# Performance work log

Measured on AMD Instinct MI355X. Metric: run time of the kernel, lower is better.

The kernel has to match this reference:

```python
import jax, jax.numpy as jnp
import numpy as np

LN_EPS = 1e-5


def layer_norm(h, gamma, beta):
    m = jnp.mean(h, axis=-1, keepdims=True)
    v = jnp.mean((h - m) ** 2, axis=-1, keepdims=True)
    return (h - m) * jax.lax.rsqrt(v + LN_EPS) * gamma + beta


def setup_inputs() -> dict:
    key = jax.random.key(0)
    ks = jax.random.split(key, 4)
    B, N, D, H = 4, 256, 256, 256
    x = jax.random.normal(ks[0], (B, N, D), dtype=jnp.float32)
    # Linear(2D, H): weight stored as (in, out) for x @ W
    Wg = jax.random.normal(ks[1], (2 * D, H), dtype=jnp.float32) * (1.0 / np.sqrt(2 * D))
    bg = jnp.zeros((H,), dtype=jnp.float32)
    g_gamma = jnp.ones((H,), dtype=jnp.float32)
    g_beta = jnp.zeros((H,), dtype=jnp.float32)
    Wf = jax.random.normal(ks[2], (H, H), dtype=jnp.float32) * (1.0 / np.sqrt(H))
    bf = jnp.zeros((H,), dtype=jnp.float32)
    f_gamma = jnp.ones((H,), dtype=jnp.float32)
    f_beta = jnp.zeros((H,), dtype=jnp.float32)
    return {"x": x, "Wg": Wg, "bg": bg, "g_gamma": g_gamma, "g_beta": g_beta,
            "Wf": Wf, "bf": bf, "f_gamma": f_gamma, "f_beta": f_beta}


def reference(x, Wg, bg, g_gamma, g_beta, Wf, bf, f_gamma, f_beta):
    B, N, D = x.shape
    # Linear on concat([xi, xj]) == xi @ Wg[:D] + xj @ Wg[D:] ; avoids the (B,N,N,2D) cat.
    a = jnp.einsum('bnd,dh->bnh', x, Wg[:D])   # i-part
    b = jnp.einsum('bnd,dh->bnh', x, Wg[D:])   # j-part
    # pair pre-activation: (B, N_i, N_j, H)
    pre = a[:, :, None, :] + b[:, None, :, :] + bg
    r = layer_norm(jax.nn.relu(pre), g_gamma, g_beta)
    r = jnp.sum(r, axis=(1, 2))                # (B, H)
    rel = layer_norm(jax.nn.relu(r @ Wf + bf), f_gamma, f_beta)  # (B, H)
    return rel[:, None, :] + x                 # broadcast over N
```

## Files before the change

### kernel.cpp

```cpp
#include <hip/hip_runtime.h>

#define LN_EPS 1e-5f

constexpr int Bn = 4, Nn = 256, Dn = 256, Hn = 256;

__global__ __launch_bounds__(256) void gemm_ab_kernel(
    const float* __restrict__ x, const float* __restrict__ Wg,
    const float* __restrict__ bg, float* __restrict__ aA, float* __restrict__ bB)
{
    int mt = blockIdx.x;
    int half = blockIdx.y;
    int m0 = mt * 8;
    int t = threadIdx.x;
    __shared__ float xs[8][256];
    const float4* xsrc = reinterpret_cast<const float4*>(x + m0 * Dn);
    float4* xdst = reinterpret_cast<float4*>(&xs[0][0]);
    for (int k = t; k < 512; k += 256) xdst[k] = xsrc[k];
    __syncthreads();
    int h = t;
    const float* W = Wg + (half ? Dn * Hn : 0) + h;
    float acc[8];
    float binit = half ? 0.0f : bg[h];
#pragma unroll
    for (int mm = 0; mm < 8; ++mm) acc[mm] = binit;
    for (int d = 0; d < 256; d += 4) {
        float w0 = W[(d + 0) * Hn];
        float w1 = W[(d + 1) * Hn];
        float w2 = W[(d + 2) * Hn];
        float w3 = W[(d + 3) * Hn];
#pragma unroll
        for (int mm = 0; mm < 8; ++mm) {
            float4 xv = *reinterpret_cast<const float4*>(&xs[mm][d]);
            acc[mm] = fmaf(xv.x, w0, acc[mm]);
            acc[mm] = fmaf(xv.y, w1, acc[mm]);
            acc[mm] = fmaf(xv.z, w2, acc[mm]);
            acc[mm] = fmaf(xv.w, w3, acc[mm]);
        }
    }
    float* outp = half ? bB : aA;
#pragma unroll
    for (int mm = 0; mm < 8; ++mm) outp[(m0 + mm) * Hn + h] = acc[mm];
}

__global__ __launch_bounds__(512) void pair_kernel(
    const float* __restrict__ aA, const float* __restrict__ bB,
    float* __restrict__ part)
{
    int b  = blockIdx.x >> 6;
    int i0 = (blockIdx.x & 63) * 4;
    int t = threadIdx.x;
    __shared__ float A[4][256];
    __shared__ float2 invd[4][256];

    for (int k = t; k < 1024; k += 512)
        A[k >> 8][k & 255] = aA[(b * Nn + i0 + (k >> 8)) * Hn + (k & 255)];
    __syncthreads();

    int j = t & 255;
    int g = t >> 8;

    {
        float s0 = 0.f, s1 = 0.f, q0 = 0.f, q1 = 0.f;
        const float* brow = bB + (b * Nn + j) * Hn;
        const float* A0 = A[2 * g];
        const float* A1 = A[2 * g + 1];
#pragma unroll 2
        for (int h = 0; h < 256; h += 4) {
            float4 bb = *reinterpret_cast<const float4*>(brow + h);
            float4 a0 = *reinterpret_cast<const float4*>(A0 + h);
            float4 a1 = *reinterpret_cast<const float4*>(A1 + h);
            float v;
            v = fmaxf(a0.x + bb.x, 0.f); s0 += v; q0 = fmaf(v, v, q0);
            v = fmaxf(a0.y + bb.y, 0.f); s0 += v; q0 = fmaf(v, v, q0);
            v = fmaxf(a0.z + bb.z, 0.f); s0 += v; q0 = fmaf(v, v, q0);
            v = fmaxf(a0.w + bb.w, 0.f); s0 += v; q0 = fmaf(v, v, q0);
            v = fmaxf(a1.x + bb.x, 0.f); s1 += v; q1 = fmaf(v, v, q1);
            v = fmaxf(a1.y + bb.y, 0.f); s1 += v; q1 = fmaf(v, v, q1);
            v = fmaxf(a1.z + bb.z, 0.f); s1 += v; q1 = fmaf(v, v, q1);
            v = fmaxf(a1.w + bb.w, 0.f); s1 += v; q1 = fmaf(v, v, q1);
        }
        float m0 = s0 * (1.f / 256.f);
        float m1 = s1 * (1.f / 256.f);
        float inv0 = rsqrtf(q0 * (1.f / 256.f) - m0 * m0 + LN_EPS);
        float inv1 = rsqrtf(q1 * (1.f / 256.f) - m1 * m1 + LN_EPS);
        invd[2 * g][j]     = make_float2(inv0, -m0 * inv0);
        invd[2 * g + 1][j] = make_float2(inv1, -m1 * inv1);
    }
    __syncthreads();

    int h = t & 255;
    float a0 = A[2 * g][h];
    float a1 = A[2 * g + 1][h];
    float acc0 = 0.f, acc1 = 0.f;
    const float* bcol = bB + b * Nn * Hn + h;
#pragma unroll 4
    for (int j2 = 0; j2 < 256; ++j2) {
        float bb = bcol[j2 * Hn];
        float2 id0 = invd[2 * g][j2];
        float2 id1 = invd[2 * g + 1][j2];
        float v0 = fmaxf(a0 + bb, 0.f);
        float v1 = fmaxf(a1 + bb, 0.f);
        acc0 += fmaf(id0.x, v0, id0.y);
        acc1 += fmaf(id1.x, v1, id1.y);
    }
    part[(b * Nn + i0 + 2 * g) * Hn + h]     = acc0;
    part[(b * Nn + i0 + 2 * g + 1) * Hn + h] = acc1;
}

__global__ __launch_bounds__(1024) void finish_kernel(
    const float* __restrict__ part,
    const float* __restrict__ gg, const float* __restrict__ gb,
    const float* __restrict__ Wf, const float* __restrict__ bfv,
    const float* __restrict__ fg, const float* __restrict__ fb,
    float* __restrict__ rel)
{
    int b = blockIdx.x;
    int t = threadIdx.x;
    int h = t & 255;
    int q = t >> 8;

    __shared__ float psum[4][256];
    __shared__ float rs[256];
    __shared__ float ysum[4][256];
    __shared__ float pS[16], pQ[16];

    float s = 0.f;
    const float* p = part + (b * Nn + q * 64) * Hn + h;
#pragma unroll 4
    for (int i = 0; i < 64; ++i) s += p[i * Hn];
    psum[q][h] = s;
    __syncthreads();

    if (q == 0) {
        float rsum = psum[0][h] + psum[1][h] + psum[2][h] + psum[3][h];
        rs[h] = gg[h] * rsum + 65536.0f * gb[h];
    }
    __syncthreads();

    float y = 0.f;
    const float* Wcol = Wf + (q * 64) * Hn + h;
#pragma unroll 4
    for (int k = 0; k < 64; ++k) y = fmaf(rs[q * 64 + k], Wcol[k * Hn], y);
    ysum[q][h] = y;
    __syncthreads();

    float v = fmaxf(ysum[0][h] + ysum[1][h] + ysum[2][h] + ysum[3][h] + bfv[h], 0.f);

    float sv = v, qv = v * v;
#pragma unroll
    for (int off = 32; off >= 1; off >>= 1) {
        sv += __shfl_xor(sv, off, 64);
        qv += __shfl_xor(qv, off, 64);
    }
    int wid = t >> 6, lane = t & 63;
    if (lane == 0) { pS[wid] = sv; pQ[wid] = qv; }
    __syncthreads();
    float S = 0.f, Q = 0.f;
#pragma unroll
    for (int w = 0; w < 16; ++w) { S += pS[w]; Q += pQ[w]; }
    float m = S * (1.f / 1024.f);
    float var = Q * (1.f / 1024.f) - m * m;
    float inv = rsqrtf(var + LN_EPS);

    if (q == 0)
        rel[b * Hn + h] = (v - m) * inv * fg[h] + fb[h];
}

__global__ __launch_bounds__(256) void add_kernel(
    const float* __restrict__ rel, const float* __restrict__ x,
    float* __restrict__ out)
{
    int idx = blockIdx.x * blockDim.x + threadIdx.x;
    int b = idx >> 14;
    int d4 = idx & 63;
    float4 r4 = reinterpret_cast<const float4*>(rel)[b * 64 + d4];
    float4 x4 = reinterpret_cast<const float4*>(x)[idx];
    float4 o;
    o.x = r4.x + x4.x;
    o.y = r4.y + x4.y;
    o.z = r4.z + x4.z;
    o.w = r4.w + x4.w;
    reinterpret_cast<float4*>(out)[idx] = o;
}

extern "C" void kernel_launch(void* const* d_in, const int* in_sizes, int n_in,
                              void* d_out, int out_size, void* d_ws, size_t ws_size,
                              hipStream_t stream)
{
    const float* x   = (const float*)d_in[0];
    const float* Wg  = (const float*)d_in[1];
    const float* bg  = (const float*)d_in[2];
    const float* gg  = (const float*)d_in[3];
    const float* gb  = (const float*)d_in[4];
    const float* Wf  = (const float*)d_in[5];
    const float* bfv = (const float*)d_in[6];
    const float* fg  = (const float*)d_in[7];
    const float* fb  = (const float*)d_in[8];
    float* out = (float*)d_out;

    float* ws   = (float*)d_ws;
    float* aA   = ws;
    float* bB   = ws + 262144;
    float* part = ws + 524288;
    float* rel  = ws + 786432;

    gemm_ab_kernel<<<dim3(128, 2), 256, 0, stream>>>(x, Wg, bg, aA, bB);
    pair_kernel<<<256, 512, 0, stream>>>(aA, bB, part);
    finish_kernel<<<4, 1024, 0, stream>>>(part, gg, gb, Wf, bfv, fg, fb, rel);
    add_kernel<<<256, 256, 0, stream>>>(rel, x, out);
}
```

Before: 125.5 us.

## Transpose b into workspace, atomically reduce pair sums, shrink GEMM tiles

The GEMM kernel now also writes a transposed copy of b, so the pair kernel's per-j statistics pass reads b with coalesced column-major loads instead of strided rows. The per-pair LayerNorm offset term is folded into a single per-batch scalar accumulated with atomics. Per-block partial sums are atomically added into a small reduction buffer, replacing the large partial array that finish_kernel had to reduce. The GEMM tile is halved to 4 rows to double the block count, and the inner loop is unrolled by 8. This trades an extra strided write of b in the GEMM and atomic contention for less memory traffic and less finish work. It also relies on gemm block 0 zeroing the accumulator before later kernels run, and float atomics make the summation order nondeterministic.

```diff
diff --git a/kernel.cpp b/kernel.cpp
--- a/kernel.cpp
+++ b/kernel.cpp
@@ -3,54 +3,76 @@
 #define LN_EPS 1e-5f
 
 constexpr int Bn = 4, Nn = 256, Dn = 256, Hn = 256;
+
 
 __global__ __launch_bounds__(256) void gemm_ab_kernel(
     const float* __restrict__ x, const float* __restrict__ Wg,
-    const float* __restrict__ bg, float* __restrict__ aA, float* __restrict__ bB)
+    const float* __restrict__ bg, float* __restrict__ aA,
+    float* __restrict__ bB, float* __restrict__ bBt, float* __restrict__ rC)
 {
     int mt = blockIdx.x;
     int half = blockIdx.y;
-    int m0 = mt * 8;
+    int m0 = mt * 4;
     int t = threadIdx.x;
-    __shared__ float xs[8][256];
+
+    if (mt == 0 && half == 0) {
+        for (int k = t; k < 1028; k += 256) rC[k] = 0.0f;
+    }
+
+    __shared__ float xs[4][256];
     const float4* xsrc = reinterpret_cast<const float4*>(x + m0 * Dn);
-    float4* xdst = reinterpret_cast<float4*>(&xs[0][0]);
-    for (int k = t; k < 512; k += 256) xdst[k] = xsrc[k];
-    __syncthreads();
+    reinterpret_cast<float4*>(&xs[0][0])[t] = xsrc[t];
+    __syncthreads();
+
     int h = t;
     const float* W = Wg + (half ? Dn * Hn : 0) + h;
-    float acc[8];
     float binit = half ? 0.0f : bg[h];
-#pragma unroll
-    for (int mm = 0; mm < 8; ++mm) acc[mm] = binit;
-    for (int d = 0; d < 256; d += 4) {
+    float acc[4] = {binit, binit, binit, binit};
+
+    for (int d = 0; d < 256; d += 8) {
         float w0 = W[(d + 0) * Hn];
         float w1 = W[(d + 1) * Hn];
         float w2 = W[(d + 2) * Hn];
         float w3 = W[(d + 3) * Hn];
-#pragma unroll
-        for (int mm = 0; mm < 8; ++mm) {
-            float4 xv = *reinterpret_cast<const float4*>(&xs[mm][d]);
-            acc[mm] = fmaf(xv.x, w0, acc[mm]);
-            acc[mm] = fmaf(xv.y, w1, acc[mm]);
-            acc[mm] = fmaf(xv.z, w2, acc[mm]);
-            acc[mm] = fmaf(xv.w, w3, acc[mm]);
+        float w4 = W[(d + 4) * Hn];
+        float w5 = W[(d + 5) * Hn];
+        float w6 = W[(d + 6) * Hn];
+        float w7 = W[(d + 7) * Hn];
+#pragma unroll
+        for (int mm = 0; mm < 4; ++mm) {
+            float4 xa = *reinterpret_cast<const float4*>(&xs[mm][d]);
+            float4 xb = *reinterpret_cast<const float4*>(&xs[mm][d + 4]);
+            float a = acc[mm];
+            a = fmaf(xa.x, w0, a); a = fmaf(xa.y, w1, a);
+            a = fmaf(xa.z, w2, a); a = fmaf(xa.w, w3, a);
+            a = fmaf(xb.x, w4, a); a = fmaf(xb.y, w5, a);
+            a = fmaf(xb.z, w6, a); a = fmaf(xb.w, w7, a);
+            acc[mm] = a;
         }
     }
-    float* outp = half ? bB : aA;
-#pragma unroll
-    for (int mm = 0; mm < 8; ++mm) outp[(m0 + mm) * Hn + h] = acc[mm];
+
+    if (half == 0) {
+#pragma unroll
+        for (int mm = 0; mm < 4; ++mm) aA[(m0 + mm) * Hn + h] = acc[mm];
+    } else {
+#pragma unroll
+        for (int mm = 0; mm < 4; ++mm) bB[(m0 + mm) * Hn + h] = acc[mm];
+        int b = m0 >> 8, i0 = m0 & 255;
+        float4 v = make_float4(acc[0], acc[1], acc[2], acc[3]);
+        *reinterpret_cast<float4*>(&bBt[(b * Hn + h) * Nn + i0]) = v;
+    }
 }
 
 __global__ __launch_bounds__(512) void pair_kernel(
     const float* __restrict__ aA, const float* __restrict__ bB,
-    float* __restrict__ part)
+    const float* __restrict__ bBt, float* __restrict__ rC)
 {
     int b  = blockIdx.x >> 6;
     int i0 = (blockIdx.x & 63) * 4;
     int t = threadIdx.x;
     __shared__ float A[4][256];
-    __shared__ float2 invd[4][256];
+    __shared__ float invL[4][256];
+    __shared__ float red[2][256];
 
     for (int k = t; k < 1024; k += 512)
         A[k >> 8][k & 255] = aA[(b * Nn + i0 + (k >> 8)) * Hn + (k & 255)];
@@ -61,30 +83,37 @@
 
     {
         float s0 = 0.f, s1 = 0.f, q0 = 0.f, q1 = 0.f;
-        const float* brow = bB + (b * Nn + j) * Hn;
+        const float* bt = bBt + b * Hn * Nn + j;
         const float* A0 = A[2 * g];
         const float* A1 = A[2 * g + 1];
 #pragma unroll 2
         for (int h = 0; h < 256; h += 4) {
-            float4 bb = *reinterpret_cast<const float4*>(brow + h);
             float4 a0 = *reinterpret_cast<const float4*>(A0 + h);
             float4 a1 = *reinterpret_cast<const float4*>(A1 + h);
+            float b0 = bt[(h + 0) << 8];
+            float b1 = bt[(h + 1) << 8];
+            float b2 = bt[(h + 2) << 8];
+            float b3 = bt[(h + 3) << 8];
             float v;
-            v = fmaxf(a0.x + bb.x, 0.f); s0 += v; q0 = fmaf(v, v, q0);
-            v = fmaxf(a0.y + bb.y, 0.f); s0 += v; q0 = fmaf(v, v, q0);
-            v = fmaxf(a0.z + bb.z, 0.f); s0 += v; q0 = fmaf(v, v, q0);
-            v = fmaxf(a0.w + bb.w, 0.f); s0 += v; q0 = fmaf(v, v, q0);
-            v = fmaxf(a1.x + bb.x, 0.f); s1 += v; q1 = fmaf(v, v, q1);
-            v = fmaxf(a1.y + bb.y, 0.f); s1 += v; q1 = fmaf(v, v, q1);
-            v = fmaxf(a1.z + bb.z, 0.f); s1 += v; q1 = fmaf(v, v, q1);
-            v = fmaxf(a1.w + bb.w, 0.f); s1 += v; q1 = fmaf(v, v, q1);
+            v = fmaxf(a0.x + b0, 0.f); s0 += v; q0 = fmaf(v, v, q0);
+            v = fmaxf(a0.y + b1, 0.f); s0 += v; q0 = fmaf(v, v, q0);
+            v = fmaxf(a0.z + b2, 0.f); s0 += v; q0 = fmaf(v, v, q0);
+            v = fmaxf(a0.w + b3, 0.f); s0 += v; q0 = fmaf(v, v, q0);
+            v = fmaxf(a1.x + b0, 0.f); s1 += v; q1 = fmaf(v, v, q1);
+            v = fmaxf(a1.y + b1, 0.f); s1 += v; q1 = fmaf(v, v, q1);
+            v = fmaxf(a1.z + b2, 0.f); s1 += v; q1 = fmaf(v, v, q1);
+            v = fmaxf(a1.w + b3, 0.f); s1 += v; q1 = fmaf(v, v, q1);
         }
         float m0 = s0 * (1.f / 256.f);
         float m1 = s1 * (1.f / 256.f);
         float inv0 = rsqrtf(q0 * (1.f / 256.f) - m0 * m0 + LN_EPS);
         float inv1 = rsqrtf(q1 * (1.f / 256.f) - m1 * m1 + LN_EPS);
-        invd[2 * g][j]     = make_float2(inv0, -m0 * inv0);
-        invd[2 * g + 1][j] = make_float2(inv1, -m1 * inv1);
+        invL[2 * g][j]     = inv0;
+        invL[2 * g + 1][j] = inv1;
+        float ysum = -(m0 * inv0) - (m1 * inv1);
+#pragma unroll
+        for (int off = 32; off >= 1; off >>= 1) ysum += __shfl_xor(ysum, off, 64);
+        if ((t & 63) == 0) atomicAdd(&rC[1024 + b], ysum);
     }
     __syncthreads();
 
@@ -95,20 +124,19 @@
     const float* bcol = bB + b * Nn * Hn + h;
 #pragma unroll 4
     for (int j2 = 0; j2 < 256; ++j2) {
-        float bb = bcol[j2 * Hn];
-        float2 id0 = invd[2 * g][j2];
-        float2 id1 = invd[2 * g + 1][j2];
-        float v0 = fmaxf(a0 + bb, 0.f);
-        float v1 = fmaxf(a1 + bb, 0.f);
-        acc0 += fmaf(id0.x, v0, id0.y);
-        acc1 += fmaf(id1.x, v1, id1.y);
-    }
-    part[(b * Nn + i0 + 2 * g) * Hn + h]     = acc0;
-    part[(b * Nn + i0 + 2 * g + 1) * Hn + h] = acc1;
+        float bb = bcol[j2 << 8];
+        float i0v = invL[2 * g][j2];
+        float i1v = invL[2 * g + 1][j2];
+        acc0 = fmaf(i0v, fmaxf(a0 + bb, 0.f), acc0);
+        acc1 = fmaf(i1v, fmaxf(a1 + bb, 0.f), acc1);
+    }
+    red[g][h] = acc0 + acc1;
+    __syncthreads();
+    if (g == 0) atomicAdd(&rC[b * Hn + h], red[0][h] + red[1][h]);
 }
 
 __global__ __launch_bounds__(1024) void finish_kernel(
-    const float* __restrict__ part,
+    const float* __restrict__ rC,
     const float* __restrict__ gg, const float* __restrict__ gb,
     const float* __restrict__ Wf, const float* __restrict__ bfv,
     const float* __restrict__ fg, const float* __restrict__ fb,
@@ -119,27 +147,17 @@
     int h = t & 255;
     int q = t >> 8;
 
-    __shared__ float psum[4][256];
     __shared__ float rs[256];
     __shared__ float ysum[4][256];
     __shared__ float pS[16], pQ[16];
 
-    float s = 0.f;
-    const float* p = part + (b * Nn + q * 64) * Hn + h;
-#pragma unroll 4
-    for (int i = 0; i < 64; ++i) s += p[i * Hn];
-    psum[q][h] = s;
-    __syncthreads();
-
-    if (q == 0) {
-        float rsum = psum[0][h] + psum[1][h] + psum[2][h] + psum[3][h];
-        rs[h] = gg[h] * rsum + 65536.0f * gb[h];
-    }
+    if (q == 0)
+        rs[h] = gg[h] * (rC[b * Hn + h] + rC[1024 + b]) + 65536.0f * gb[h];
     __syncthreads();
 
     float y = 0.f;
     const float* Wcol = Wf + (q * 64) * Hn + h;
-#pragma unroll 4
+#pragma unroll 8
     for (int k = 0; k < 64; ++k) y = fmaf(rs[q * 64 + k], Wcol[k * Hn], y);
     ysum[q][h] = y;
     __syncthreads();
@@ -201,11 +219,12 @@
     float* ws   = (float*)d_ws;
     float* aA   = ws;
     float* bB   = ws + 262144;
-    float* part = ws + 524288;
-    float* rel  = ws + 786432;
-
-    gemm_ab_kernel<<<dim3(128, 2), 256, 0, stream>>>(x, Wg, bg, aA, bB);
-    pair_kernel<<<256, 512, 0, stream>>>(aA, bB, part);
-    finish_kernel<<<4, 1024, 0, stream>>>(part, gg, gb, Wf, bfv, fg, fb, rel);
+    float* bBt  = ws + 524288;
+    float* rC   = ws + 786432;
+    float* rel  = ws + 787712;
+
+    gemm_ab_kernel<<<dim3(256, 2), 256, 0, stream>>>(x, Wg, bg, aA, bB, bBt, rC);
+    pair_kernel<<<256, 512, 0, stream>>>(aA, bB, bBt, rC);
+    finish_kernel<<<4, 1024, 0, stream>>>(rC, gg, gb, Wf, bfv, fg, fb, rel);
     add_kernel<<<256, 256, 0, stream>>>(rel, x, out);
 }
```

Result: slower. 143.9 us (+14.7%).
